# Kernel tuning notes

Measured on AMD Instinct MI355X. Metric: run time of the kernel, lower is better.

## Reference

```python
import jax, jax.numpy as jnp
import numpy as np

B, TENC, EPROJS, DUNITS, ODIM, L, ATT_DIM = 64, 800, 512, 512, 5000, 128, 320
SOS = EOS = ODIM - 1


def setup_inputs() -> dict:
    key = jax.random.key(0)
    ks = jax.random.split(key, 16)
    s = 0.02
    D = DUNITS
    return {
        "hpad": jax.random.normal(ks[0], (B, TENC, EPROJS), jnp.float32),
        # keep lengths in [TENC//2, TENC] so every row has valid frames
        "hlen": jnp.clip(jax.random.randint(ks[1], (B,), 0, TENC + 1), TENC // 2, TENC).astype(jnp.int32),
        "ys": jax.random.randint(ks[2], (B, L), 0, ODIM - 1),  # int labels (exclude eos)
        "embed": s * jax.random.normal(ks[3], (ODIM, D), jnp.float32),
        # torch.nn.LSTMCell params: gates order (i, f, g, o)
        "W_ih0": s * jax.random.normal(ks[4], (4 * D, D + EPROJS), jnp.float32),
        "W_hh0": s * jax.random.normal(ks[5], (4 * D, D), jnp.float32),
        "b_ih0": jnp.zeros((4 * D,), jnp.float32),
        "b_hh0": jnp.zeros((4 * D,), jnp.float32),
        "W_ih1": s * jax.random.normal(ks[6], (4 * D, D), jnp.float32),
        "W_hh1": s * jax.random.normal(ks[7], (4 * D, D), jnp.float32),
        "b_ih1": jnp.zeros((4 * D,), jnp.float32),
        "b_hh1": jnp.zeros((4 * D,), jnp.float32),
        # AttDot attention projections (no bias, as in espnet mlp_enc/mlp_dec usage)
        "Wa_enc": s * jax.random.normal(ks[8], (EPROJS, ATT_DIM), jnp.float32),
        "Wa_dec": s * jax.random.normal(ks[9], (D, ATT_DIM), jnp.float32),
        "W_out": s * jax.random.normal(ks[10], (ODIM, D), jnp.float32),
        "b_out": jnp.zeros((ODIM,), jnp.float32),
    }


def _lstm_cell(x, h, c, Wi, Wh, bi, bh):
    g = x @ Wi.T + bi + h @ Wh.T + bh
    i, f, gg, o = jnp.split(g, 4, axis=-1)
    c2 = jax.nn.sigmoid(f) * c + jax.nn.sigmoid(i) * jnp.tanh(gg)
    h2 = jax.nn.sigmoid(o) * jnp.tanh(c2)
    return h2, c2


def _forward(hpad, hlen, ys, embed, W_ih0, W_hh0, b_ih0, b_hh0,
             W_ih1, W_hh1, b_ih1, b_hh1, Wa_enc, Wa_dec, W_out, b_out):
    D = DUNITS
    tmask = jnp.arange(TENC)[None, :] < hlen[:, None]          # [B, T]
    hm = hpad * tmask[:, :, None]                               # mask_by_length
    enc_pre = jnp.tanh(jnp.einsum('bte,ea->bta', hm, Wa_enc))   # [B, T, A] precomputed

    sos_col = jnp.full((B, 1), SOS, ys.dtype)
    eos_col = jnp.full((B, 1), EOS, ys.dtype)
    ys_in = jnp.concatenate([sos_col, ys], axis=1)              # [B, L+1]
    ys_out = jnp.concatenate([ys, eos_col], axis=1)             # [B, L+1]
    eys = embed[ys_in]                                          # [B, L+1, D]

    zeros = jnp.zeros((B, D), hpad.dtype)
    carry0 = (zeros, zeros, zeros, zeros)  # z0, c0, z1, c1

    def step(carry, ey_t):
        z0, c0, z1, c1 = carry
        # AttDot: e = <tanh(enc W), tanh(z0 W)> with length masking
        d = jnp.tanh(z0 @ Wa_dec)                               # [B, A]
        e = jnp.einsum('ba,bta->bt', d, enc_pre)                # [B, T]
        e = jnp.where(tmask, e, jnp.float32(-1e9))
        w = jax.nn.softmax(e, axis=-1)
        att_c = jnp.einsum('bt,bte->be', w, hm)                 # [B, eprojs]
        x = jnp.concatenate([ey_t, att_c], axis=-1)             # [B, D+eprojs]
        z0, c0 = _lstm_cell(x, z0, c0, W_ih0, W_hh0, b_ih0, b_hh0)
        z1, c1 = _lstm_cell(z0, z1, c1, W_ih1, W_hh1, b_ih1, b_hh1)
        return (z0, c0, z1, c1), z1                             # gen_feat='s' -> top hidden

    _, z_all = jax.lax.scan(step, carry0, jnp.swapaxes(eys, 0, 1))  # [L+1, B, D]
    z_all = jnp.swapaxes(z_all, 0, 1)                           # [B, L+1, D]

    logits = jnp.einsum('bld,vd->blv', z_all, W_out) + b_out    # [B, L+1, V]
    logp = jax.nn.log_softmax(logits, axis=-1)
    nll = -jnp.take_along_axis(logp, ys_out[..., None], axis=-1)[..., 0]
    # F.cross_entropy mean over all tokens (no padding here), then *= mean(len(ys_in)) - 1 = L
    loss = nll.mean() * jnp.float32(L)
    acc = (logits.argmax(-1) == ys_out).mean()
    return loss, acc


def reference(hpad, hlen, ys, embed, W_ih0, W_hh0, b_ih0, b_hh0,
              W_ih1, W_hh1, b_ih1, b_hh1, Wa_enc, Wa_dec, W_out, b_out):
    return _forward(hpad, hlen, ys, embed, W_ih0, W_hh0, b_ih0, b_hh0,
                    W_ih1, W_hh1, b_ih1, b_hh1, Wa_enc, Wa_dec, W_out, b_out)
```

## Files before the change

kernel.cpp:

```cpp
#include <hip/hip_runtime.h>
#include <math.h>

typedef unsigned short u16;
typedef unsigned char u8;
typedef float f32x4 __attribute__((ext_vector_type(4)));
typedef short s16x8 __attribute__((ext_vector_type(8)));

#define ODIM 5000
#define NROWS 8256

__device__ inline u16 f2bf(float f){
  unsigned u = __float_as_uint(f);
  return (u16)((u + 0x7FFFu + ((u >> 16) & 1u)) >> 16);
}
__device__ inline float bf2f(u16 h){ return __uint_as_float(((unsigned)h) << 16); }
__device__ inline float sigm(float x){ return 1.f/(1.f + expf(-x)); }

__device__ inline unsigned f2fp8(float f){
  unsigned u = __float_as_uint(f);
  unsigned s = (u>>24)&0x80u;
  int e = (int)((u>>23)&0xffu) - 127;
  if (e < -7) return s;
  unsigned full = (u & 0x7fffffu) | 0x800000u;
  unsigned keep = full >> 20;
  unsigned rem  = full & 0xFFFFFu;
  keep += (rem > 0x80000u) || (rem == 0x80000u && (keep & 1u));
  int te = e + 7;
  if (keep >= 16u){ keep >>= 1; te += 1; }
  if (te >= 16) return s | 0x7Eu;
  if (te < 1)  return s;
  return s | ((unsigned)te<<3) | (keep & 7u);
}
__device__ inline float fp8d(unsigned v){
  unsigned r = ((v & 0x80u) << 24) | (((v & 0x7fu) + 960u) << 20);
  return __uint_as_float(r);
}

__global__ void a0_init(float* att2, float* pd, float* z0f, float* z1f,
                        float* c0, float* c1, float* accum){
  int tid = blockIdx.x*256 + threadIdx.x, n = 64*256;
  for (int i=tid;i<2*64*516;i+=n) att2[i]=0.f;
  for (int i=tid;i<2621440;i+=n) pd[i]=0.f;
  for (int i=tid;i<32768;i+=n){ z0f[i]=0.f; z1f[i]=0.f; c0[i]=0.f; c1[i]=0.f; }
  if (tid < 8) accum[tid]=0.f;
}

__global__ void a1_wcvt(const float* waenc, const float* wadec,
  const float* wih0, const float* whh0, const float* wih1, const float* whh1,
  const float* bih0, const float* bhh0, const float* bih1, const float* bhh1,
  const float* wout,
  u16* waencT, u16* wdKC, u16* wcat0, u16* wcat1, u16* wee, u16* woutb,
  float* bc0, float* bc1)
{
  int tid = blockIdx.x*blockDim.x + threadIdx.x;
  int nth = gridDim.x*blockDim.x;
  for (int i=tid; i<320*512; i+=nth){
    int n=i>>9, k=i&511;
    waencT[i] = f2bf(waenc[k*320+n]);
    wdKC[i]   = f2bf(wadec[i]);
  }
  for (int i=tid; i<2048*1024; i+=nth){
    int np=i>>10, k=i&1023;
    int u=np>>2, g=np&3, r=g*512+u;
    wcat0[i] = f2bf(k<512 ? wih0[r*1024+512+k] : whh0[r*512+(k-512)]);
    wcat1[i] = f2bf(k<512 ? wih1[r*512+k]      : whh1[r*512+(k-512)]);
  }
  for (int i=tid; i<2048*512; i+=nth){
    int np=i>>9, k=i&511;
    int u=np>>2, g=np&3, r=g*512+u;
    wee[i] = f2bf(wih0[r*1024+k]);
  }
  for (int i=tid; i<5000*512; i+=nth) woutb[i] = f2bf(wout[i]);
  for (int i=tid; i<2048; i+=nth){
    int u=i>>2, g=i&3, r=g*512+u;
    bc0[i] = bih0[r]+bhh0[r];
    bc1[i] = bih1[r]+bhh1[r];
  }
}

__global__ __launch_bounds__(256) void a2_encpre(
  const float* __restrict__ hpad, const int* __restrict__ hlen,
  const u16* __restrict__ waencT, u8* __restrict__ hm8, u8* __restrict__ encp8)
{
  __shared__ u16 A[64][40];
  __shared__ u16 BT[320][40];
  int tid = threadIdx.x, blk = blockIdx.x;
  int wave = tid>>6, lane = tid&63;
  f32x4 acc[20];
  #pragma unroll
  for (int f=0;f<20;f++) acc[f] = (f32x4){0.f,0.f,0.f,0.f};
  int srow = tid>>2, skoff = (tid&3)*8;
  int grow_s = blk*64 + srow;
  int b_s = grow_s/800, t_s = grow_s - b_s*800;
  bool valid_s = t_s < hlen[b_s];
  for (int c=0;c<16;c++){
    int k0 = c*32;
    {
      const float* src = hpad + (size_t)grow_s*512 + k0 + skoff;
      float4 v0 = *(const float4*)(src);
      float4 v1 = *(const float4*)(src+4);
      if (!valid_s){ v0 = make_float4(0,0,0,0); v1 = make_float4(0,0,0,0); }
      *(short4*)&A[srow][skoff] = make_short4(
        (short)f2bf(v0.x),(short)f2bf(v0.y),(short)f2bf(v0.z),(short)f2bf(v0.w));
      *(short4*)&A[srow][skoff+4] = make_short4(
        (short)f2bf(v1.x),(short)f2bf(v1.y),(short)f2bf(v1.z),(short)f2bf(v1.w));
      unsigned lo = f2fp8(v0.x) | (f2fp8(v0.y)<<8) | (f2fp8(v0.z)<<16) | (f2fp8(v0.w)<<24);
      unsigned hi = f2fp8(v1.x) | (f2fp8(v1.y)<<8) | (f2fp8(v1.z)<<16) | (f2fp8(v1.w)<<24);
      *(uint2*)(hm8 + (size_t)grow_s*512 + k0 + skoff) = make_uint2(lo, hi);
    }
    for (int id=tid; id<1280; id+=256){
      int n = id>>2, kv = (id&3)*8;
      *(s16x8*)&BT[n][kv] = *(const s16x8*)(waencT + n*512 + k0 + kv);
    }
    __syncthreads();
    s16x8 av = *(const s16x8*)&A[wave*16 + (lane&15)][(lane>>4)*8];
    #pragma unroll
    for (int f=0;f<20;f++){
      s16x8 bv = *(const s16x8*)&BT[f*16+(lane&15)][(lane>>4)*8];
      acc[f] = __builtin_amdgcn_mfma_f32_16x16x32_bf16(av,bv,acc[f],0,0,0);
    }
    __syncthreads();
  }
  #pragma unroll
  for (int f=0;f<20;f++){
    int col = f*16 + (lane&15);
    #pragma unroll
    for (int r=0;r<4;r++){
      int grow = blk*64 + wave*16 + (lane>>4)*4 + r;
      encp8[(size_t)grow*320 + col] = (u8)f2fp8(tanhf(acc[f][r]));
    }
  }
}

__global__ __launch_bounds__(256) void a3_geys(
  const int* __restrict__ ys, const float* __restrict__ embed,
  const u16* __restrict__ wee, const float* __restrict__ bc0,
  u16* __restrict__ geys)
{
  __shared__ u16 A[64][88];
  __shared__ u16 BT[256][88];
  int t = blockIdx.x, nt = blockIdx.y, tid = threadIdx.x;
  int wave=tid>>6, lane=tid&63;
  f32x4 acc[16];
  #pragma unroll
  for (int f=0;f<16;f++) acc[f]=(f32x4){0.f,0.f,0.f,0.f};
  int srow = tid>>2, skoff=(tid&3)*16;
  int idx = (t==0) ? (ODIM-1) : ys[srow*128 + (t-1)];
  const float* asrc = embed + (size_t)idx*512;
  for (int c=0;c<8;c++){
    int k0=c*64;
    #pragma unroll
    for (int i=0;i<16;i+=4){
      float4 v = *(const float4*)(asrc + k0 + skoff + i);
      *(short4*)&A[srow][skoff+i] =
        make_short4((short)f2bf(v.x),(short)f2bf(v.y),(short)f2bf(v.z),(short)f2bf(v.w));
    }
    for (int id=tid; id<2048; id+=256){
      int n = id>>3, kv=(id&7)*8;
      *(s16x8*)&BT[n][kv] = *(const s16x8*)(wee + (size_t)(nt*256+n)*512 + k0 + kv);
    }
    __syncthreads();
    #pragma unroll
    for (int kk=0;kk<64;kk+=32){
      s16x8 av = *(const s16x8*)&A[wave*16+(lane&15)][kk+(lane>>4)*8];
      #pragma unroll
      for (int f=0;f<16;f++){
        s16x8 bv = *(const s16x8*)&BT[f*16+(lane&15)][kk+(lane>>4)*8];
        acc[f] = __builtin_amdgcn_mfma_f32_16x16x32_bf16(av,bv,acc[f],0,0,0);
      }
    }
    __syncthreads();
  }
  #pragma unroll
  for (int f=0;f<16;f++){
    int colL = f*16+(lane&15);
    int gc = nt*256+colL;
    float bb = bc0[gc];
    #pragma unroll
    for (int r=0;r<4;r++){
      int row = wave*16 + (lane>>4)*4 + r;
      geys[(size_t)(t*64+row)*2048 + gc] = f2bf(acc[f][r] + bb);
    }
  }
}

__global__ __launch_bounds__(256) void k1p(
  int t,
  const u8* __restrict__ encp8, const u8* __restrict__ hm8, const int* __restrict__ hlen,
  const float* __restrict__ pd,
  const u16* __restrict__ wcat1, const float* __restrict__ bc1,
  const u16* __restrict__ z0b, u16* __restrict__ z1b, float* __restrict__ c1,
  u16* __restrict__ zall, float* __restrict__ att)
{
  __shared__ __align__(16) char smem[25600];
  const int blk = blockIdx.x, tid = threadIdx.x;
  const int wave = tid>>6, lane = tid&63;
  const int p2 = (t+1)&1;

  if (blk < 512){
    int b = blk>>3, ch = blk&7;
    float* attp = att + ((t&1)*64*516);
    float* attl = (float*)smem;
    float* sl   = (float*)(smem+8192);
    float* dl   = (float*)(smem+8224);
    {
      const float* q0 = pd + (size_t)p2*1310720 + (size_t)b*320;
      for (int col=tid; col<320; col+=256){
        const float* q = q0 + col;
        float a0=0.f,a1=0.f,a2=0.f,a3=0.f,a4=0.f,a5=0.f,a6=0.f,a7=0.f;
        #pragma unroll
        for (int s=0;s<64;s+=8){
          a0 += q[(size_t)(s+0)*20480];
          a1 += q[(size_t)(s+1)*20480];
          a2 += q[(size_t)(s+2)*20480];
          a3 += q[(size_t)(s+3)*20480];
          a4 += q[(size_t)(s+4)*20480];
          a5 += q[(size_t)(s+5)*20480];
          a6 += q[(size_t)(s+6)*20480];
          a7 += q[(size_t)(s+7)*20480];
        }
        dl[col] = tanhf(((a0+a1)+(a2+a3))+((a4+a5)+(a6+a7)));
      }
    }
    __syncthreads();
    float dreg[8];
    #pragma unroll
    for (int j=0;j<8;j++) dreg[j] = (lane<40) ? dl[lane*8+j] : 0.f;
    float attacc[8];
    #pragma unroll
    for (int j=0;j<8;j++) attacc[j]=0.f;
    float sacc = 0.f;
    int len = hlen[b];
    int t0 = ch*100;
    int tend = t0+100 < len ? t0+100 : len;
    for (int i0 = t0 + wave; i0 < tend; i0 += 16){
      uint2 ea[4], ha[4];
      #pragma unroll
      for (int q=0;q<4;q++){
        int tt = i0 + 4*q;
        if (tt < tend){
          if (lane<40) ea[q] = *(const uint2*)(encp8 + (size_t)(b*800+tt)*320 + lane*8);
          ha[q] = *(const uint2*)(hm8 + (size_t)(b*800+tt)*512 + lane*8);
        }
      }
      #pragma unroll
      for (int q=0;q<4;q++){
        int tt = i0 + 4*q;
        if (tt < tend){
          float e = 0.f;
          if (lane<40){
            unsigned w0 = ea[q].x, w1 = ea[q].y;
            e += dreg[0]*fp8d(w0&0xffu) + dreg[1]*fp8d((w0>>8)&0xffu)
               + dreg[2]*fp8d((w0>>16)&0xffu) + dreg[3]*fp8d(w0>>24);
            e += dreg[4]*fp8d(w1&0xffu) + dreg[5]*fp8d((w1>>8)&0xffu)
               + dreg[6]*fp8d((w1>>16)&0xffu) + dreg[7]*fp8d(w1>>24);
          }
          #pragma unroll
          for (int off=32; off; off>>=1) e += __shfl_xor(e, off);
          float pw = expf(fminf(e, 60.f));
          sacc += pw;
          unsigned h0 = ha[q].x, h1 = ha[q].y;
          attacc[0] += pw*fp8d(h0&0xffu);
          attacc[1] += pw*fp8d((h0>>8)&0xffu);
          attacc[2] += pw*fp8d((h0>>16)&0xffu);
          attacc[3] += pw*fp8d(h0>>24);
          attacc[4] += pw*fp8d(h1&0xffu);
          attacc[5] += pw*fp8d((h1>>8)&0xffu);
          attacc[6] += pw*fp8d((h1>>16)&0xffu);
          attacc[7] += pw*fp8d(h1>>24);
        }
      }
    }
    __syncthreads();
    #pragma unroll
    for (int j=0;j<8;j++) attl[wave*512 + lane*8+j] = attacc[j];
    if (lane==0) sl[wave] = sacc;
    __syncthreads();
    for (int c2 = tid; c2 < 512; c2 += 256){
      float v = attl[c2]+attl[512+c2]+attl[1024+c2]+attl[1536+c2];
      atomicAdd(&attp[b*516 + c2], v);
    }
    if (tid==0) atomicAdd(&attp[b*516 + 512], sl[0]+sl[1]+sl[2]+sl[3]);
  } else {
    if (t < 1) return;
    int nb = blk - 512;
    const u16* z0n = z0b + p2*64*512;
    const u16* z1p = z1b + ((p2^1)*64*512);
    u16* z1n = z1b + p2*64*512;
    u16* zallt = zall + (size_t)(t-1)*64*512;
    u16 (*A)[88]  = (u16(*)[88])smem;
    u16 (*BT)[88] = (u16(*)[88])(smem+11264);
    f32x4 acc[2];
    acc[0]=(f32x4){0.f,0.f,0.f,0.f}; acc[1]=(f32x4){0.f,0.f,0.f,0.f};
    int srow=tid>>2, skoff=(tid&3)*16;
    int brow=tid>>3, bkoff=(tid&7)*8;
    for (int c=0;c<16;c++){
      int k0=c*64;
      const u16* asrc = (c<8) ? (z0n + srow*512 + k0 + skoff)
                              : (z1p + srow*512 + (k0-512) + skoff);
      *(s16x8*)&A[srow][skoff]   = *(const s16x8*)asrc;
      *(s16x8*)&A[srow][skoff+8] = *(const s16x8*)(asrc+8);
      *(s16x8*)&BT[brow][bkoff] = *(const s16x8*)(wcat1 + (size_t)(nb*32+brow)*1024 + k0 + bkoff);
      __syncthreads();
      #pragma unroll
      for (int kk=0;kk<64;kk+=32){
        s16x8 av = *(const s16x8*)&A[wave*16+(lane&15)][kk+(lane>>4)*8];
        #pragma unroll
        for (int f=0;f<2;f++){
          s16x8 bv = *(const s16x8*)&BT[f*16+(lane&15)][kk+(lane>>4)*8];
          acc[f] = __builtin_amdgcn_mfma_f32_16x16x32_bf16(av,bv,acc[f],0,0,0);
        }
      }
      __syncthreads();
    }
    float (*gl)[36] = (float(*)[36])smem;
    #pragma unroll
    for (int f=0;f<2;f++){
      int colL = f*16+(lane&15);
      float bb = bc1[nb*32+colL];
      #pragma unroll
      for (int r=0;r<4;r++){
        int rowL = wave*16+(lane>>4)*4+r;
        gl[rowL][colL] = acc[f][r] + bb;
      }
    }
    __syncthreads();
    for (int it=tid; it<512; it+=256){
      int bb=it>>3, ul=it&7;
      float gi=gl[bb][ul*4], gf=gl[bb][ul*4+1], gg=gl[bb][ul*4+2], go=gl[bb][ul*4+3];
      int ug = nb*8+ul;
      float cp = c1[bb*512+ug];
      float cn = sigm(gf)*cp + sigm(gi)*tanhf(gg);
      float z = sigm(go)*tanhf(cn);
      c1[bb*512+ug]=cn;
      u16 zb = f2bf(z);
      z1n[bb*512+ug]=zb;
      zallt[bb*512+ug]=zb;
    }
  }
}

__global__ __launch_bounds__(256) void k2p(
  const float* __restrict__ attp, float* __restrict__ attz,
  const u16* __restrict__ z0p, u16* __restrict__ z0n,
  float* __restrict__ c0,
  const u16* __restrict__ wcat0, const u16* __restrict__ geyt,
  const u16* __restrict__ wdKC, float* __restrict__ pdout)
{
  __shared__ __align__(16) char smem[16896];
  __shared__ float sinv[64];
  __shared__ float zsl[512];
  __shared__ u16 wsl[2560];
  u16 (*A)[88]  = (u16(*)[88])smem;
  u16 (*BT)[88] = (u16(*)[88])(smem+11264);
  int tid = threadIdx.x, nb = blockIdx.x;
  int wave=tid>>6, lane=tid&63;
  if (tid < 64) sinv[tid] = 1.f/attp[tid*516+512];
  for (int id=tid; id<320; id+=256)
    *(s16x8*)&wsl[id*8] = *(const s16x8*)(wdKC + nb*2560 + id*8);
  __syncthreads();
  f32x4 acc[2];
  acc[0]=(f32x4){0.f,0.f,0.f,0.f}; acc[1]=(f32x4){0.f,0.f,0.f,0.f};
  int srow=tid>>2, skoff=(tid&3)*16;
  int brow=tid>>3, bkoff=(tid&7)*8;
  for (int c=0;c<16;c++){
    int k0=c*64;
    if (c<8){
      const float* src = attp + srow*516 + k0 + skoff;
      float sv = sinv[srow];
      #pragma unroll
      for (int i=0;i<16;i+=4){
        float4 v = *(const float4*)(src+i);
        *(short4*)&A[srow][skoff+i] = make_short4(
          (short)f2bf(v.x*sv),(short)f2bf(v.y*sv),(short)f2bf(v.z*sv),(short)f2bf(v.w*sv));
      }
    } else {
      const u16* src = z0p + srow*512 + (k0-512) + skoff;
      *(s16x8*)&A[srow][skoff]   = *(const s16x8*)(src);
      *(s16x8*)&A[srow][skoff+8] = *(const s16x8*)(src+8);
    }
    *(s16x8*)&BT[brow][bkoff] = *(const s16x8*)(wcat0 + (size_t)(nb*32+brow)*1024 + k0 + bkoff);
    __syncthreads();
    #pragma unroll
    for (int kk=0;kk<64;kk+=32){
      s16x8 av = *(const s16x8*)&A[wave*16+(lane&15)][kk+(lane>>4)*8];
      #pragma unroll
      for (int f=0;f<2;f++){
        s16x8 bv = *(const s16x8*)&BT[f*16+(lane&15)][kk+(lane>>4)*8];
        acc[f] = __builtin_amdgcn_mfma_f32_16x16x32_bf16(av,bv,acc[f],0,0,0);
      }
    }
    __syncthreads();
  }
  float (*gl)[36] = (float(*)[36])smem;
  #pragma unroll
  for (int f=0;f<2;f++){
    int colL = f*16+(lane&15);
    #pragma unroll
    for (int r=0;r<4;r++){
      int rowL = wave*16+(lane>>4)*4+r;
      gl[rowL][colL] = acc[f][r] + bf2f(geyt[rowL*2048 + nb*32 + colL]);
    }
  }
  __syncthreads();
  for (int it=tid; it<512; it+=256){
    int bb=it>>3, ul=it&7;
    float gi=gl[bb][ul*4], gf=gl[bb][ul*4+1], gg=gl[bb][ul*4+2], go=gl[bb][ul*4+3];
    int ug = nb*8+ul;
    float cp = c0[bb*512+ug];
    float cn = sigm(gf)*cp + sigm(gi)*tanhf(gg);
    float z = sigm(go)*tanhf(cn);
    c0[bb*512+ug]=cn;
    z0n[bb*512+ug]=f2bf(z);
    zsl[it] = z;
  }
  __syncthreads();
  for (int idx=tid; idx<20480; idx+=256){
    int b = idx/320, col = idx - b*320;
    float a = 0.f;
    #pragma unroll
    for (int ul=0; ul<8; ul++)
      a += zsl[b*8+ul]*bf2f(wsl[ul*320+col]);
    pdout[(size_t)nb*20480 + idx] = a;
  }
  for (int i=tid + nb*256; i < 64*516; i += 64*256) attz[i] = 0.f;
}

__global__ __launch_bounds__(256) void kf_cell1(
  const u16* __restrict__ z0n, const u16* __restrict__ z1p,
  u16* __restrict__ z1n, float* __restrict__ c1,
  const u16* __restrict__ wcat1, const float* __restrict__ bc1,
  u16* __restrict__ zallt)
{
  __shared__ __align__(16) char smem[25600];
  int tid = threadIdx.x, wave=tid>>6, lane=tid&63;
  int nb = blockIdx.x;
  u16 (*A)[88]  = (u16(*)[88])smem;
  u16 (*BT)[88] = (u16(*)[88])(smem+11264);
  f32x4 acc[2];
  acc[0]=(f32x4){0.f,0.f,0.f,0.f}; acc[1]=(f32x4){0.f,0.f,0.f,0.f};
  int srow=tid>>2, skoff=(tid&3)*16;
  int brow=tid>>3, bkoff=(tid&7)*8;
  for (int c=0;c<16;c++){
    int k0=c*64;
    const u16* asrc = (c<8) ? (z0n + srow*512 + k0 + skoff)
                            : (z1p + srow*512 + (k0-512) + skoff);
    *(s16x8*)&A[srow][skoff]   = *(const s16x8*)asrc;
    *(s16x8*)&A[srow][skoff+8] = *(const s16x8*)(asrc+8);
    *(s16x8*)&BT[brow][bkoff] = *(const s16x8*)(wcat1 + (size_t)(nb*32+brow)*1024 + k0 + bkoff);
    __syncthreads();
    #pragma unroll
    for (int kk=0;kk<64;kk+=32){
      s16x8 av = *(const s16x8*)&A[wave*16+(lane&15)][kk+(lane>>4)*8];
      #pragma unroll
      for (int f=0;f<2;f++){
        s16x8 bv = *(const s16x8*)&BT[f*16+(lane&15)][kk+(lane>>4)*8];
        acc[f] = __builtin_amdgcn_mfma_f32_16x16x32_bf16(av,bv,acc[f],0,0,0);
      }
    }
    __syncthreads();
  }
  float (*gl)[36] = (float(*)[36])smem;
  #pragma unroll
  for (int f=0;f<2;f++){
    int colL = f*16+(lane&15);
    float bb = bc1[nb*32+colL];
    #pragma unroll
    for (int r=0;r<4;r++){
      int rowL = wave*16+(lane>>4)*4+r;
      gl[rowL][colL] = acc[f][r] + bb;
    }
  }
  __syncthreads();
  for (int it=tid; it<512; it+=256){
    int bb=it>>3, ul=it&7;
    float gi=gl[bb][ul*4], gf=gl[bb][ul*4+1], gg=gl[bb][ul*4+2], go=gl[bb][ul*4+3];
    int ug = nb*8+ul;
    float cp = c1[bb*512+ug];
    float cn = sigm(gf)*cp + sigm(gi)*tanhf(gg);
    float z = sigm(go)*tanhf(cn);
    c1[bb*512+ug]=cn;
    u16 zb = f2bf(z);
    z1n[bb*512+ug]=zb;
    zallt[bb*512+ug]=zb;
  }
}

__global__ __launch_bounds__(512) void k4_logits(
  const u16* __restrict__ zall, const u16* __restrict__ woutb,
  const float* __restrict__ b_out, const int* __restrict__ ys,
  float* __restrict__ partials)
{
  __shared__ char smem[46080];
  u16 (*A)[40]  = (u16(*)[40])smem;
  u16 (*BT)[40] = (u16(*)[40])(smem + 5120);
  int t = blockIdx.x, v = blockIdx.y;
  int tid = threadIdx.x, wave = tid>>6, lane = tid&63;
  int mf = wave>>1;
  int nh = (wave&1)*256;
  f32x4 acc[16];
  #pragma unroll
  for (int f=0;f<16;f++) acc[f]=(f32x4){0.f,0.f,0.f,0.f};
  for (int c=0;c<16;c++){
    int k0 = c*32;
    { int row = tid>>3, koff=(tid&7)*4;
      *(short4*)&A[row][koff] = *(const short4*)(zall + (size_t)(t*64+row)*512 + k0 + koff); }
    { int n = v*512 + tid;
      if (n < ODIM){
        const u16* src = woutb + (size_t)n*512 + k0;
        #pragma unroll
        for (int i=0;i<32;i+=8) *(s16x8*)&BT[tid][i] = *(const s16x8*)(src+i);
      } else {
        s16x8 z = 0;
        #pragma unroll
        for (int i=0;i<32;i+=8) *(s16x8*)&BT[tid][i] = z;
      }
    }
    __syncthreads();
    s16x8 av = *(const s16x8*)&A[mf*16 + (lane&15)][(lane>>4)*8];
    #pragma unroll
    for (int f=0;f<16;f++){
      s16x8 bv = *(const s16x8*)&BT[nh + f*16 + (lane&15)][(lane>>4)*8];
      acc[f] = __builtin_amdgcn_mfma_f32_16x16x32_bf16(av,bv,acc[f],0,0,0);
    }
    __syncthreads();
  }
  float (*ll)[518] = (float(*)[518])smem;
  for (int g=0; g<4; g++){
    if (mf == g){
      #pragma unroll
      for (int f=0;f<16;f++){
        int colL = nh + f*16 + (lane&15);
        int gcol = v*512 + colL;
        float bo = (gcol < ODIM) ? b_out[gcol] : 0.f;
        #pragma unroll
        for (int r=0;r<4;r++){
          int rowL = (lane>>4)*4 + r;
          ll[rowL][colL] = acc[f][r] + bo;
        }
      }
    }
    __syncthreads();
    int r = tid>>5, j = tid&31;
    float m = -1e30f, s = 0.f, amax = -1e30f; int aidx = 0;
    #pragma unroll
    for (int i=0;i<16;i++){
      int cL = j + 32*i;
      int gc = v*512 + cL;
      if (gc < ODIM){
        float val = ll[r][cL];
        if (val > m){ s = s*expf(m-val) + 1.f; m = val; }
        else s += expf(val - m);
        if (val > amax){ amax = val; aidx = gc; }
      }
    }
    #pragma unroll
    for (int off=16; off; off>>=1){
      float mo = __shfl_xor(m, off), so = __shfl_xor(s, off);
      float ao = __shfl_xor(amax, off); int io = __shfl_xor(aidx, off);
      float M = fmaxf(m, mo);
      s = s*expf(m-M) + so*expf(mo-M);
      m = M;
      if (ao > amax || (ao == amax && io < aidx)){ amax = ao; aidx = io; }
    }
    if (j == 0){
      int b = g*16 + r;
      int grow = t*64 + b;
      int lab = (t < 128) ? ys[b*128 + t] : (ODIM-1);
      float labval = 0.f, labf = 0.f;
      int lo = lab - v*512;
      if (lo >= 0 && lo < 512){ labval = ll[r][lo]; labf = 1.f; }
      float* pp = partials + (size_t)(grow*10 + v)*8;
      pp[0]=m; pp[1]=s; pp[2]=amax; pp[3]=__int_as_float(aidx); pp[4]=labval; pp[5]=labf;
    }
    __syncthreads();
  }
}

__global__ __launch_bounds__(256) void k5_loss(
  const float* __restrict__ partials, const int* __restrict__ ys, float* accum)
{
  int row = blockIdx.x*256 + threadIdx.x;
  float nll = 0.f; int corr = 0;
  if (row < NROWS){
    float M=-1e30f, S=0.f, amax=-1e30f, labval=0.f; int aidx=0;
    for (int v=0;v<10;v++){
      const float* pp = partials + (size_t)(row*10+v)*8;
      float m=pp[0], s=pp[1], a=pp[2]; int ai=__float_as_int(pp[3]);
      float MM = fmaxf(M, m);
      S = S*expf(M-MM) + s*expf(m-MM);
      M = MM;
      if (a > amax || (a == amax && ai < aidx)){ amax=a; aidx=ai; }
      if (pp[5] != 0.f) labval = pp[4];
    }
    nll = M + logf(S) - labval;
    int t = row>>6, b = row&63;
    int lab = (t < 128) ? ys[b*128+t] : (ODIM-1);
    corr = (aidx == lab) ? 1 : 0;
  }
  __shared__ float sn[256]; __shared__ int sc[256];
  sn[threadIdx.x]=nll; sc[threadIdx.x]=corr; __syncthreads();
  for (int st=128; st; st>>=1){
    if (threadIdx.x<st){ sn[threadIdx.x]+=sn[threadIdx.x+st]; sc[threadIdx.x]+=sc[threadIdx.x+st]; }
    __syncthreads();
  }
  if (threadIdx.x==0){
    atomicAdd(accum, sn[0]);
    atomicAdd((int*)accum + 1, sc[0]);
  }
}

__global__ void k6_final(const float* accum, float* out){
  out[0] = accum[0]/(float)NROWS * 128.f;
  out[1] = (float)(((const int*)accum)[1])/(float)NROWS;
}

extern "C" void kernel_launch(void* const* d_in, const int* in_sizes, int n_in,
                              void* d_out, int out_size, void* d_ws, size_t ws_size,
                              hipStream_t stream)
{
  const float* hpad  = (const float*)d_in[0];
  const int*   hlen  = (const int*)d_in[1];
  const int*   ys    = (const int*)d_in[2];
  const float* embed = (const float*)d_in[3];
  const float* wih0  = (const float*)d_in[4];
  const float* whh0  = (const float*)d_in[5];
  const float* bih0  = (const float*)d_in[6];
  const float* bhh0  = (const float*)d_in[7];
  const float* wih1  = (const float*)d_in[8];
  const float* whh1  = (const float*)d_in[9];
  const float* bih1  = (const float*)d_in[10];
  const float* bhh1  = (const float*)d_in[11];
  const float* waenc = (const float*)d_in[12];
  const float* wadec = (const float*)d_in[13];
  const float* wout  = (const float*)d_in[14];
  const float* bout  = (const float*)d_in[15];

  char* ws = (char*)d_ws;
  u8*    hm8     = (u8*)(ws + 0);
  u8*    encp8   = (u8*)(ws + 26214400);
  u16*   waencT  = (u16*)(ws + 42598400);
  u16*   wdKC    = (u16*)(ws + 42926080);
  u16*   wcat0   = (u16*)(ws + 43253760);
  u16*   wcat1   = (u16*)(ws + 47448064);
  u16*   wee     = (u16*)(ws + 51642368);
  u16*   woutb   = (u16*)(ws + 53739520);
  float* bc0     = (float*)(ws + 58859520);
  float* bc1     = (float*)(ws + 58867712);
  u16*   geys    = (u16*)(ws + 58875904);
  float* pd      = (float*)(ws + 92692480);
  float* att     = (float*)(ws + 103178240);
  u16*   z0b     = (u16*)(ws + 103442432);
  u16*   z1b     = (u16*)(ws + 103573504);
  float* c0      = (float*)(ws + 103704576);
  float* c1      = (float*)(ws + 103835648);
  u16*   zall    = (u16*)(ws + 103966720);
  float* partials= (float*)(ws + 112420864);
  float* accum   = (float*)(ws + 115062784);

  a0_init<<<64,256,0,stream>>>(att, pd, (float*)z0b, (float*)z1b, c0, c1, accum);
  a1_wcvt<<<512,256,0,stream>>>(waenc, wadec, wih0, whh0, wih1, whh1,
                                bih0, bhh0, bih1, bhh1, wout,
                                waencT, wdKC, wcat0, wcat1, wee, woutb, bc0, bc1);
  a2_encpre<<<800,256,0,stream>>>(hpad, hlen, waencT, hm8, encp8);
  a3_geys<<<dim3(129,8),256,0,stream>>>(ys, embed, wee, bc0, geys);

  for (int t=0; t<129; t++){
    int p = t & 1, q = p^1;
    k1p<<<576,256,0,stream>>>(t, encp8, hm8, hlen, pd, wcat1, bc1,
                              z0b, z1b, c1, zall, att);
    k2p<<<64,256,0,stream>>>(att + p*64*516, att + q*64*516,
                             z0b + q*64*512, z0b + p*64*512,
                             c0, wcat0, geys + (size_t)t*64*2048,
                             wdKC, pd + (size_t)p*1310720);
  }
  kf_cell1<<<64,256,0,stream>>>(z0b, z1b + 64*512, z1b, c1, wcat1, bc1,
                                zall + (size_t)128*64*512);

  k4_logits<<<dim3(129,10),512,0,stream>>>(zall, woutb, bout, ys, partials);
  k5_loss<<<33,256,0,stream>>>(partials, ys, accum);
  k6_final<<<1,1,0,stream>>>(accum, (float*)d_out);
}
```

Before: 7.775 ms.

## Store encoder activations in bf16 and widen k2p blocks to 128 gate columns

Replaces the fp8 e4m3 storage of the masked encoder states and the attention pre-activations with bf16, and drops the software fp8 encode/decode in the attention loop. Separately, the per-step cell-0 kernel now runs 16 blocks, each computing 128 gate columns (32 units) instead of 64 blocks of 32. This cuts the decoder-projection partial sums from 64 to 16 slices, so k1p reduces fewer partials. In exchange, the attention pass reads twice as many bytes per frame every step, and the recurrent step uses far fewer workgroups, each doing more serial work. The pd buffer also now shares its workspace offset with partials.

```diff
diff --git a/kernel.cpp b/kernel.cpp
--- a/kernel.cpp
+++ b/kernel.cpp
@@ -2,7 +2,6 @@
 #include <math.h>
 
 typedef unsigned short u16;
-typedef unsigned char u8;
 typedef float f32x4 __attribute__((ext_vector_type(4)));
 typedef short s16x8 __attribute__((ext_vector_type(8)));
 
@@ -15,32 +14,12 @@
 }
 __device__ inline float bf2f(u16 h){ return __uint_as_float(((unsigned)h) << 16); }
 __device__ inline float sigm(float x){ return 1.f/(1.f + expf(-x)); }
-
-__device__ inline unsigned f2fp8(float f){
-  unsigned u = __float_as_uint(f);
-  unsigned s = (u>>24)&0x80u;
-  int e = (int)((u>>23)&0xffu) - 127;
-  if (e < -7) return s;
-  unsigned full = (u & 0x7fffffu) | 0x800000u;
-  unsigned keep = full >> 20;
-  unsigned rem  = full & 0xFFFFFu;
-  keep += (rem > 0x80000u) || (rem == 0x80000u && (keep & 1u));
-  int te = e + 7;
-  if (keep >= 16u){ keep >>= 1; te += 1; }
-  if (te >= 16) return s | 0x7Eu;
-  if (te < 1)  return s;
-  return s | ((unsigned)te<<3) | (keep & 7u);
-}
-__device__ inline float fp8d(unsigned v){
-  unsigned r = ((v & 0x80u) << 24) | (((v & 0x7fu) + 960u) << 20);
-  return __uint_as_float(r);
-}
 
 __global__ void a0_init(float* att2, float* pd, float* z0f, float* z1f,
                         float* c0, float* c1, float* accum){
   int tid = blockIdx.x*256 + threadIdx.x, n = 64*256;
   for (int i=tid;i<2*64*516;i+=n) att2[i]=0.f;
-  for (int i=tid;i<2621440;i+=n) pd[i]=0.f;
+  for (int i=tid;i<655360;i+=n) pd[i]=0.f;
   for (int i=tid;i<32768;i+=n){ z0f[i]=0.f; z1f[i]=0.f; c0[i]=0.f; c1[i]=0.f; }
   if (tid < 8) accum[tid]=0.f;
 }
@@ -80,7 +59,7 @@
 
 __global__ __launch_bounds__(256) void a2_encpre(
   const float* __restrict__ hpad, const int* __restrict__ hlen,
-  const u16* __restrict__ waencT, u8* __restrict__ hm8, u8* __restrict__ encp8)
+  const u16* __restrict__ waencT, u16* __restrict__ hm, u16* __restrict__ encp)
 {
   __shared__ u16 A[64][40];
   __shared__ u16 BT[320][40];
@@ -100,13 +79,12 @@
       float4 v0 = *(const float4*)(src);
       float4 v1 = *(const float4*)(src+4);
       if (!valid_s){ v0 = make_float4(0,0,0,0); v1 = make_float4(0,0,0,0); }
-      *(short4*)&A[srow][skoff] = make_short4(
-        (short)f2bf(v0.x),(short)f2bf(v0.y),(short)f2bf(v0.z),(short)f2bf(v0.w));
-      *(short4*)&A[srow][skoff+4] = make_short4(
-        (short)f2bf(v1.x),(short)f2bf(v1.y),(short)f2bf(v1.z),(short)f2bf(v1.w));
-      unsigned lo = f2fp8(v0.x) | (f2fp8(v0.y)<<8) | (f2fp8(v0.z)<<16) | (f2fp8(v0.w)<<24);
-      unsigned hi = f2fp8(v1.x) | (f2fp8(v1.y)<<8) | (f2fp8(v1.z)<<16) | (f2fp8(v1.w)<<24);
-      *(uint2*)(hm8 + (size_t)grow_s*512 + k0 + skoff) = make_uint2(lo, hi);
+      short4 p0 = make_short4((short)f2bf(v0.x),(short)f2bf(v0.y),(short)f2bf(v0.z),(short)f2bf(v0.w));
+      short4 p1 = make_short4((short)f2bf(v1.x),(short)f2bf(v1.y),(short)f2bf(v1.z),(short)f2bf(v1.w));
+      *(short4*)&A[srow][skoff]   = p0;
+      *(short4*)&A[srow][skoff+4] = p1;
+      *(short4*)(hm + (size_t)grow_s*512 + k0 + skoff)     = p0;
+      *(short4*)(hm + (size_t)grow_s*512 + k0 + skoff + 4) = p1;
     }
     for (int id=tid; id<1280; id+=256){
       int n = id>>2, kv = (id&3)*8;
@@ -127,7 +105,7 @@
     #pragma unroll
     for (int r=0;r<4;r++){
       int grow = blk*64 + wave*16 + (lane>>4)*4 + r;
-      encp8[(size_t)grow*320 + col] = (u8)f2fp8(tanhf(acc[f][r]));
+      encp[(size_t)grow*320 + col] = f2bf(tanhf(acc[f][r]));
     }
   }
 }
@@ -186,7 +164,7 @@
 
 __global__ __launch_bounds__(256) void k1p(
   int t,
-  const u8* __restrict__ encp8, const u8* __restrict__ hm8, const int* __restrict__ hlen,
+  const u16* __restrict__ encp, const u16* __restrict__ hm, const int* __restrict__ hlen,
   const float* __restrict__ pd,
   const u16* __restrict__ wcat1, const float* __restrict__ bc1,
   const u16* __restrict__ z0b, u16* __restrict__ z1b, float* __restrict__ c1,
@@ -204,22 +182,18 @@
     float* sl   = (float*)(smem+8192);
     float* dl   = (float*)(smem+8224);
     {
-      const float* q0 = pd + (size_t)p2*1310720 + (size_t)b*320;
+      const float* q0 = pd + (size_t)p2*327680 + (size_t)b*320;
       for (int col=tid; col<320; col+=256){
         const float* q = q0 + col;
-        float a0=0.f,a1=0.f,a2=0.f,a3=0.f,a4=0.f,a5=0.f,a6=0.f,a7=0.f;
+        float a0=0.f,a1=0.f,a2=0.f,a3=0.f;
         #pragma unroll
-        for (int s=0;s<64;s+=8){
+        for (int s=0;s<16;s+=4){
           a0 += q[(size_t)(s+0)*20480];
           a1 += q[(size_t)(s+1)*20480];
           a2 += q[(size_t)(s+2)*20480];
           a3 += q[(size_t)(s+3)*20480];
-          a4 += q[(size_t)(s+4)*20480];
-          a5 += q[(size_t)(s+5)*20480];
-          a6 += q[(size_t)(s+6)*20480];
-          a7 += q[(size_t)(s+7)*20480];
         }
-        dl[col] = tanhf(((a0+a1)+(a2+a3))+((a4+a5)+(a6+a7)));
+        dl[col] = tanhf((a0+a1)+(a2+a3));
       }
     }
     __syncthreads();
@@ -234,13 +208,13 @@
     int t0 = ch*100;
     int tend = t0+100 < len ? t0+100 : len;
     for (int i0 = t0 + wave; i0 < tend; i0 += 16){
-      uint2 ea[4], ha[4];
+      s16x8 ev[4], hv[4];
       #pragma unroll
       for (int q=0;q<4;q++){
         int tt = i0 + 4*q;
         if (tt < tend){
-          if (lane<40) ea[q] = *(const uint2*)(encp8 + (size_t)(b*800+tt)*320 + lane*8);
-          ha[q] = *(const uint2*)(hm8 + (size_t)(b*800+tt)*512 + lane*8);
+          if (lane<40) ev[q] = *(const s16x8*)(encp + (size_t)(b*800+tt)*320 + lane*8);
+          hv[q] = *(const s16x8*)(hm + (size_t)(b*800+tt)*512 + lane*8);
         }
       }
       #pragma unroll
@@ -249,25 +223,15 @@
         if (tt < tend){
           float e = 0.f;
           if (lane<40){
-            unsigned w0 = ea[q].x, w1 = ea[q].y;
-            e += dreg[0]*fp8d(w0&0xffu) + dreg[1]*fp8d((w0>>8)&0xffu)
-               + dreg[2]*fp8d((w0>>16)&0xffu) + dreg[3]*fp8d(w0>>24);
-            e += dreg[4]*fp8d(w1&0xffu) + dreg[5]*fp8d((w1>>8)&0xffu)
-               + dreg[6]*fp8d((w1>>16)&0xffu) + dreg[7]*fp8d(w1>>24);
+            #pragma unroll
+            for (int j=0;j<8;j++) e += dreg[j]*bf2f((u16)ev[q][j]);
           }
           #pragma unroll
           for (int off=32; off; off>>=1) e += __shfl_xor(e, off);
           float pw = expf(fminf(e, 60.f));
           sacc += pw;
-          unsigned h0 = ha[q].x, h1 = ha[q].y;
-          attacc[0] += pw*fp8d(h0&0xffu);
-          attacc[1] += pw*fp8d((h0>>8)&0xffu);
-          attacc[2] += pw*fp8d((h0>>16)&0xffu);
-          attacc[3] += pw*fp8d(h0>>24);
-          attacc[4] += pw*fp8d(h1&0xffu);
-          attacc[5] += pw*fp8d((h1>>8)&0xffu);
-          attacc[6] += pw*fp8d((h1>>16)&0xffu);
-          attacc[7] += pw*fp8d(h1>>24);
+          #pragma unroll
+          for (int j=0;j<8;j++) attacc[j] += pw*bf2f((u16)hv[q][j]);
         }
       }
     }
@@ -347,22 +311,23 @@
   const u16* __restrict__ wcat0, const u16* __restrict__ geyt,
   const u16* __restrict__ wdKC, float* __restrict__ pdout)
 {
-  __shared__ __align__(16) char smem[16896];
+  __shared__ __align__(16) char smem[33792];
   __shared__ float sinv[64];
-  __shared__ float zsl[512];
-  __shared__ u16 wsl[2560];
+  __shared__ float zsl[2048];
+  __shared__ u16 wsl[10240];
   u16 (*A)[88]  = (u16(*)[88])smem;
   u16 (*BT)[88] = (u16(*)[88])(smem+11264);
   int tid = threadIdx.x, nb = blockIdx.x;
   int wave=tid>>6, lane=tid&63;
   if (tid < 64) sinv[tid] = 1.f/attp[tid*516+512];
-  for (int id=tid; id<320; id+=256)
-    *(s16x8*)&wsl[id*8] = *(const s16x8*)(wdKC + nb*2560 + id*8);
+  for (int id=tid; id<1280; id+=256)
+    *(s16x8*)&wsl[id*8] = *(const s16x8*)(wdKC + (size_t)nb*10240 + id*8);
   __syncthreads();
-  f32x4 acc[2];
-  acc[0]=(f32x4){0.f,0.f,0.f,0.f}; acc[1]=(f32x4){0.f,0.f,0.f,0.f};
+  f32x4 acc[8];
+  #pragma unroll
+  for (int f=0;f<8;f++) acc[f]=(f32x4){0.f,0.f,0.f,0.f};
   int srow=tid>>2, skoff=(tid&3)*16;
-  int brow=tid>>3, bkoff=(tid&7)*8;
+  int brow=tid>>1, bkoff=(tid&1)*32;
   for (int c=0;c<16;c++){
     int k0=c*64;
     if (c<8){
@@ -379,39 +344,43 @@
       *(s16x8*)&A[srow][skoff]   = *(const s16x8*)(src);
       *(s16x8*)&A[srow][skoff+8] = *(const s16x8*)(src+8);
     }
-    *(s16x8*)&BT[brow][bkoff] = *(const s16x8*)(wcat0 + (size_t)(nb*32+brow)*1024 + k0 + bkoff);
+    {
+      const u16* bsrc = wcat0 + (size_t)(nb*128+brow)*1024 + k0 + bkoff;
+      #pragma unroll
+      for (int i=0;i<32;i+=8) *(s16x8*)&BT[brow][bkoff+i] = *(const s16x8*)(bsrc+i);
+    }
     __syncthreads();
     #pragma unroll
     for (int kk=0;kk<64;kk+=32){
       s16x8 av = *(const s16x8*)&A[wave*16+(lane&15)][kk+(lane>>4)*8];
       #pragma unroll
-      for (int f=0;f<2;f++){
+      for (int f=0;f<8;f++){
         s16x8 bv = *(const s16x8*)&BT[f*16+(lane&15)][kk+(lane>>4)*8];
         acc[f] = __builtin_amdgcn_mfma_f32_16x16x32_bf16(av,bv,acc[f],0,0,0);
       }
     }
     __syncthreads();
   }
-  float (*gl)[36] = (float(*)[36])smem;
-  #pragma unroll
-  for (int f=0;f<2;f++){
+  float (*gl)[132] = (float(*)[132])smem;
+  #pragma unroll
+  for (int f=0;f<8;f++){
     int colL = f*16+(lane&15);
     #pragma unroll
     for (int r=0;r<4;r++){
-      int rowL = wave*16+(lane>>4)*4+r;
-      gl[rowL][colL] = acc[f][r] + bf2f(geyt[rowL*2048 + nb*32 + colL]);
+      int rowL = wave*16 + (lane>>4)*4 + r;
+      gl[rowL][colL] = acc[f][r] + bf2f(geyt[rowL*2048 + nb*128 + colL]);
     }
   }
   __syncthreads();
-  for (int it=tid; it<512; it+=256){
-    int bb=it>>3, ul=it&7;
-    float gi=gl[bb][ul*4], gf=gl[bb][ul*4+1], gg=gl[bb][ul*4+2], go=gl[bb][ul*4+3];
-    int ug = nb*8+ul;
-    float cp = c0[bb*512+ug];
+  for (int it=tid; it<2048; it+=256){
+    int b=it>>5, ul=it&31;
+    float gi=gl[b][ul*4], gf=gl[b][ul*4+1], gg=gl[b][ul*4+2], go=gl[b][ul*4+3];
+    int ug = nb*32+ul;
+    float cp = c0[b*512+ug];
     float cn = sigm(gf)*cp + sigm(gi)*tanhf(gg);
     float z = sigm(go)*tanhf(cn);
-    c0[bb*512+ug]=cn;
-    z0n[bb*512+ug]=f2bf(z);
+    c0[b*512+ug]=cn;
+    z0n[b*512+ug]=f2bf(z);
     zsl[it] = z;
   }
   __syncthreads();
@@ -419,11 +388,11 @@
     int b = idx/320, col = idx - b*320;
     float a = 0.f;
     #pragma unroll
-    for (int ul=0; ul<8; ul++)
-      a += zsl[b*8+ul]*bf2f(wsl[ul*320+col]);
+    for (int ul=0; ul<32; ul++)
+      a += zsl[b*32+ul]*bf2f(wsl[ul*320+col]);
     pdout[(size_t)nb*20480 + idx] = a;
   }
-  for (int i=tid + nb*256; i < 64*516; i += 64*256) attz[i] = 0.f;
+  for (int i=tid + nb*256; i < 64*516; i += 16*256) attz[i] = 0.f;
 }
 
 __global__ __launch_bounds__(256) void kf_cell1(
@@ -637,42 +606,42 @@
   const float* bout  = (const float*)d_in[15];
 
   char* ws = (char*)d_ws;
-  u8*    hm8     = (u8*)(ws + 0);
-  u8*    encp8   = (u8*)(ws + 26214400);
-  u16*   waencT  = (u16*)(ws + 42598400);
-  u16*   wdKC    = (u16*)(ws + 42926080);
-  u16*   wcat0   = (u16*)(ws + 43253760);
-  u16*   wcat1   = (u16*)(ws + 47448064);
-  u16*   wee     = (u16*)(ws + 51642368);
-  u16*   woutb   = (u16*)(ws + 53739520);
-  float* bc0     = (float*)(ws + 58859520);
-  float* bc1     = (float*)(ws + 58867712);
-  u16*   geys    = (u16*)(ws + 58875904);
-  float* pd      = (float*)(ws + 92692480);
-  float* att     = (float*)(ws + 103178240);
-  u16*   z0b     = (u16*)(ws + 103442432);
-  u16*   z1b     = (u16*)(ws + 103573504);
-  float* c0      = (float*)(ws + 103704576);
-  float* c1      = (float*)(ws + 103835648);
-  u16*   zall    = (u16*)(ws + 103966720);
-  float* partials= (float*)(ws + 112420864);
-  float* accum   = (float*)(ws + 115062784);
+  u16*   hm      = (u16*)(ws + 0);
+  u16*   encp    = (u16*)(ws + 52428800);
+  u16*   waencT  = (u16*)(ws + 85196800);
+  u16*   wdKC    = (u16*)(ws + 85524480);
+  u16*   wcat0   = (u16*)(ws + 85852160);
+  u16*   wcat1   = (u16*)(ws + 90046464);
+  u16*   wee     = (u16*)(ws + 94240768);
+  u16*   woutb   = (u16*)(ws + 96337920);
+  float* bc0     = (float*)(ws + 101457920);
+  float* bc1     = (float*)(ws + 101466112);
+  u16*   geys    = (u16*)(ws + 101474304);
+  float* att     = (float*)(ws + 135331840);
+  u16*   z0b     = (u16*)(ws + 135596032);
+  u16*   z1b     = (u16*)(ws + 135727104);
+  float* c0      = (float*)(ws + 135858176);
+  float* c1      = (float*)(ws + 135989248);
+  u16*   zall    = (u16*)(ws + 136120320);
+  float* pd      = (float*)(ws + 144574464);
+  float* partials= (float*)(ws + 144574464);
+  float* accum   = (float*)(ws + 147216384);
 
   a0_init<<<64,256,0,stream>>>(att, pd, (float*)z0b, (float*)z1b, c0, c1, accum);
   a1_wcvt<<<512,256,0,stream>>>(waenc, wadec, wih0, whh0, wih1, whh1,
                                 bih0, bhh0, bih1, bhh1, wout,
                                 waencT, wdKC, wcat0, wcat1, wee, woutb, bc0, bc1);
-  a2_encpre<<<800,256,0,stream>>>(hpad, hlen, waencT, hm8, encp8);
+  a2_encpre<<<800,256,0,stream>>>(hpad, hlen, waencT, hm, encp);
   a3_geys<<<dim3(129,8),256,0,stream>>>(ys, embed, wee, bc0, geys);
 
   for (int t=0; t<129; t++){
     int p = t & 1, q = p^1;
-    k1p<<<576,256,0,stream>>>(t, encp8, hm8, hlen, pd, wcat1, bc1,
+    k1p<<<576,256,0,stream>>>(t, encp, hm, hlen, pd, wcat1, bc1,
                               z0b, z1b, c1, zall, att);
-    k2p<<<64,256,0,stream>>>(att + p*64*516, att + q*64*516,
+    k2p<<<16,256,0,stream>>>(att + p*64*516, att + q*64*516,
                              z0b + q*64*512, z0b + p*64*512,
                              c0, wcat0, geys + (size_t)t*64*2048,
-                             wdKC, pd + (size_t)p*1310720);
+                             wdKC, pd + (size_t)p*327680);
   }
   kf_cell1<<<64,256,0,stream>>>(z0b, z1b + 64*512, z1b, c1, wcat1, bc1,
                                 zall + (size_t)128*64*512);
```

After: 9.924 ms. +27.6%, slower.
